# Kernel tuning notes

Hardware: AMD Instinct MI355X
Metric: run time of the kernel (lower is better)

Reference implementation:

```python
import jax, jax.numpy as jnp
import numpy as np

S, B, E = 512, 512, 768

def setup_inputs() -> dict:
    key = jax.random.key(0)
    k1, k2, k3 = jax.random.split(key, 3)
    inputs = jax.random.normal(k1, (S, B, E), dtype=jnp.float32)
    rotation_params = jax.random.normal(k2, (E, E), dtype=jnp.float32)
    entangle_params = jax.random.normal(k3, (E, E), dtype=jnp.float32)
    return {"inputs": inputs, "rotation_params": rotation_params, "entangle_params": entangle_params}

def reference(inputs, rotation_params, entangle_params):
    seq_len, batch, embed_dim = inputs.shape
    # Q/K projections: (S,B,E) @ (E,E) -> (S,B,E)
    q = jnp.einsum('sbe,ef->sbf', inputs, rotation_params.reshape(embed_dim, -1))
    k = jnp.einsum('sbe,ef->sbf', inputs, entangle_params.reshape(embed_dim, -1))
    v = inputs
    # Faithful to the torch code: matmul batches over seq_len, so attention
    # mixes across the BATCH axis -> scores shape (S, B, B).
    scale = 1.0 / jnp.sqrt(jnp.float32(embed_dim))
    scores = jax.nn.softmax(jnp.einsum('sbe,sce->sbc', q, k) * scale, axis=-1)
    return jnp.einsum('sbc,sce->sbe', scores, v)
```

## Files before the change

### kernel.cpp

```cpp
#include <hip/hip_runtime.h>
#include <hip/hip_bf16.h>
#include <math.h>

typedef unsigned short ushort_t;
typedef __attribute__((ext_vector_type(8))) short bf16x8;
typedef __attribute__((ext_vector_type(4))) float f32x4;

#define SCALE 0.03608439182435161f

__device__ __forceinline__ ushort_t f2bf(float f) {
  unsigned u = __float_as_uint(f);
  return (ushort_t)((u + 0x7FFFu + ((u >> 16) & 1u)) >> 16);
}
__device__ __forceinline__ float bf2f(ushort_t h) {
  return __uint_as_float(((unsigned)h) << 16);
}

__device__ __forceinline__ void split4(float4 v, ushort_t* hh, ushort_t* ll) {
  __hip_bfloat162 h01 = __float22bfloat162_rn(make_float2(v.x, v.y));
  __hip_bfloat162 h23 = __float22bfloat162_rn(make_float2(v.z, v.w));
  unsigned u01 = *(unsigned*)&h01, u23 = *(unsigned*)&h23;
  float l0 = v.x - __uint_as_float((u01 & 0xFFFFu) << 16);
  float l1 = v.y - __uint_as_float(u01 & 0xFFFF0000u);
  float l2 = v.z - __uint_as_float((u23 & 0xFFFFu) << 16);
  float l3 = v.w - __uint_as_float(u23 & 0xFFFF0000u);
  __hip_bfloat162 g01 = __float22bfloat162_rn(make_float2(l0, l1));
  __hip_bfloat162 g23 = __float22bfloat162_rn(make_float2(l2, l3));
  *(unsigned*)&hh[0] = u01; *(unsigned*)&hh[2] = u23;
  *(unsigned*)&ll[0] = *(unsigned*)&g01; *(unsigned*)&ll[2] = *(unsigned*)&g23;
}

struct MMP {
  const float* Af;  long aLd;
  const float* Bf;
  const ushort_t* Bhi; const ushort_t* Blo; long bLd;
  ushort_t* Chi; ushort_t* Clo; long cLd;
  int zMode;
  int K;
};

template <int BM>
__global__ __launch_bounds__(256) void mm(MMP P)
{
  __shared__ ushort_t lds[16384];
  ushort_t* Ah = lds;
  ushort_t* Al = lds + 4096;
  ushort_t* Bh = lds + 8192;
  ushort_t* Bl = lds + 12288;

  const int tid = threadIdx.x;
  int bx = blockIdx.x, by = blockIdx.y;
  {
    int nwg = gridDim.x * gridDim.y;
    if ((nwg & 7) == 0) {
      int id = by * gridDim.x + bx;
      int q = nwg >> 3;
      int wid = (id & 7) * q + (id >> 3);
      bx = wid % gridDim.x;
      by = wid / gridDim.x;
    }
  }
  const int m0 = by * 128, n0 = bx * 128;

  const int lane = tid & 63;
  const int wave = tid >> 6;
  const int wm = (wave >> 1) * 64, wn = (wave & 1) * 64;
  const int lr = lane & 15, g = lane >> 4;

  f32x4 acc[4][4];
  #pragma unroll
  for (int i = 0; i < 4; ++i)
    #pragma unroll
    for (int j = 0; j < 4; ++j) {
      f32x4 zv = {0.f, 0.f, 0.f, 0.f};
      acc[i][j] = zv;
    }

  for (int k0 = 0; k0 < P.K; k0 += 32) {
    #pragma unroll
    for (int rep = 0; rep < 4; ++rep) {
      int idx = tid + rep * 256;
      int row = idx >> 3, q = idx & 7;
      float4 v = *(const float4*)(P.Af + (long)(m0 + row) * P.aLd + k0 + q * 4);
      int off = row * 32 + (((q >> 1) ^ ((row >> 1) & 3)) << 3) + ((q & 1) << 2);
      ushort_t hh[4], ll[4];
      split4(v, hh, ll);
      *(uint2*)(Ah + off) = *(uint2*)hh;
      *(uint2*)(Al + off) = *(uint2*)ll;
    }
    if constexpr (BM == 0) {
      #pragma unroll
      for (int rep = 0; rep < 4; ++rep) {
        int idx = tid + rep * 256;
        int row = idx >> 3, q = idx & 7;
        float4 v = *(const float4*)(P.Bf + (long)(n0 + row) * P.bLd + k0 + q * 4);
        int off = row * 32 + (((q >> 1) ^ ((row >> 1) & 3)) << 3) + ((q & 1) << 2);
        ushort_t hh[4], ll[4];
        split4(v, hh, ll);
        *(uint2*)(Bh + off) = *(uint2*)hh;
        *(uint2*)(Bl + off) = *(uint2*)ll;
      }
    } else {
      #pragma unroll
      for (int rep = 0; rep < 2; ++rep) {
        int idx = tid + rep * 256;
        int row = idx >> 2, h8 = idx & 3;
        int off = row * 32 + ((h8 ^ ((row >> 1) & 3)) << 3);
        long gsrc = (long)(n0 + row) * P.bLd + k0 + h8 * 8;
        *(uint4*)(Bh + off) = *(const uint4*)(P.Bhi + gsrc);
        *(uint4*)(Bl + off) = *(const uint4*)(P.Blo + gsrc);
      }
    }
    __syncthreads();

    bf16x8 ar[4], br[4];
    #pragma unroll
    for (int i = 0; i < 4; ++i) {
      int row = wm + i * 16 + lr;
      ar[i] = *(const bf16x8*)(Ah + row * 32 + ((g ^ ((row >> 1) & 3)) << 3));
    }
    #pragma unroll
    for (int j = 0; j < 4; ++j) {
      int row = wn + j * 16 + lr;
      br[j] = *(const bf16x8*)(Bh + row * 32 + ((g ^ ((row >> 1) & 3)) << 3));
    }
    #pragma unroll
    for (int i = 0; i < 4; ++i)
      #pragma unroll
      for (int j = 0; j < 4; ++j)
        acc[i][j] = __builtin_amdgcn_mfma_f32_16x16x32_bf16(ar[i], br[j], acc[i][j], 0, 0, 0);
    #pragma unroll
    for (int j = 0; j < 4; ++j) {
      int row = wn + j * 16 + lr;
      bf16x8 blv = *(const bf16x8*)(Bl + row * 32 + ((g ^ ((row >> 1) & 3)) << 3));
      #pragma unroll
      for (int i = 0; i < 4; ++i)
        acc[i][j] = __builtin_amdgcn_mfma_f32_16x16x32_bf16(ar[i], blv, acc[i][j], 0, 0, 0);
    }
    #pragma unroll
    for (int i = 0; i < 4; ++i) {
      int row = wm + i * 16 + lr;
      bf16x8 alv = *(const bf16x8*)(Al + row * 32 + ((g ^ ((row >> 1) & 3)) << 3));
      #pragma unroll
      for (int j = 0; j < 4; ++j)
        acc[i][j] = __builtin_amdgcn_mfma_f32_16x16x32_bf16(alv, br[j], acc[i][j], 0, 0, 0);
    }
    __syncthreads();
  }

  #pragma unroll
  for (int i = 0; i < 4; ++i) {
    #pragma unroll
    for (int j = 0; j < 4; ++j) {
      int colG = n0 + wn + j * 16 + lr;
      #pragma unroll
      for (int r = 0; r < 4; ++r) {
        int rowG = m0 + wm + i * 16 + g * 4 + r;
        float v = acc[i][j][r];
        ushort_t hi = f2bf(v);
        ushort_t lo = f2bf(v - bf2f(hi));
        long off;
        if (P.zMode) off = (long)(rowG >> 9) * 786432 + (long)(rowG & 511) * 1536 + colG;
        else         off = (long)rowG * P.cLd + colG;
        P.Chi[off] = hi;
        P.Clo[off] = lo;
      }
    }
  }
}

__global__ __launch_bounds__(512, 2) void fsc6(ushort_t* __restrict__ slots,
                                               const float* __restrict__ X)
{
  __shared__ ushort_t lds[73728];
  float* redf = (float*)lds;
  float* reds = (float*)lds + 768;

  const int id = blockIdx.x;
  const int c = id & 7, r = id >> 3;
  const int tile = r & 7;
  const int s = c + ((r >> 3) << 3);
  const int m0 = tile * 64;

  ushort_t* Az = slots + (long)s * 786432;
  const float* Xf = X + (long)s * 393216;

  const int tid = threadIdx.x;
  const int lane = tid & 63;
  const int wave = tid >> 6;
  const int wn = wave * 64;
  const int lr = lane & 15, g = lane >> 4;

  const int ae = tid & 255;
  const int arow = ae >> 2, ah8 = ae & 3;
  const int aoff = arow * 32 + ((ah8 ^ ((arow >> 1) & 3)) << 3);
  const long asrc = (long)(m0 + arow) * 1536 + ah8 * 8 + (tid < 256 ? 0 : 768);
  const int adst = aoff + (tid < 256 ? 0 : 2048);

  f32x4 acc[4][4];
  #pragma unroll
  for (int i = 0; i < 4; ++i)
    #pragma unroll
    for (int j = 0; j < 4; ++j) {
      f32x4 zv = {0.f, 0.f, 0.f, 0.f};
      acc[i][j] = zv;
    }

  float4 bv0, bv1, bv2, bv3, bv4, bv5, bv6, bv7;
  uint4 av;

#define FSC_LOAD(K0)                                                         \
  do {                                                                       \
    av = *(const uint4*)(Az + asrc + (K0));                                  \
    const float* xb = Xf + (K0);                                             \
    bv0 = *(const float4*)(xb + (long)((tid + 0 * 512) >> 3) * 768 + ((tid + 0 * 512) & 7) * 4); \
    bv1 = *(const float4*)(xb + (long)((tid + 1 * 512) >> 3) * 768 + ((tid + 1 * 512) & 7) * 4); \
    bv2 = *(const float4*)(xb + (long)((tid + 2 * 512) >> 3) * 768 + ((tid + 2 * 512) & 7) * 4); \
    bv3 = *(const float4*)(xb + (long)((tid + 3 * 512) >> 3) * 768 + ((tid + 3 * 512) & 7) * 4); \
    bv4 = *(const float4*)(xb + (long)((tid + 4 * 512) >> 3) * 768 + ((tid + 4 * 512) & 7) * 4); \
    bv5 = *(const float4*)(xb + (long)((tid + 5 * 512) >> 3) * 768 + ((tid + 5 * 512) & 7) * 4); \
    bv6 = *(const float4*)(xb + (long)((tid + 6 * 512) >> 3) * 768 + ((tid + 6 * 512) & 7) * 4); \
    bv7 = *(const float4*)(xb + (long)((tid + 7 * 512) >> 3) * 768 + ((tid + 7 * 512) & 7) * 4); \
  } while (0)

#define FSC_WR1(BH, BL, BV, REP)                                             \
  do {                                                                       \
    int idx = tid + (REP) * 512;                                             \
    int row = idx >> 3, q = idx & 7;                                         \
    int off = row * 32 + (((q >> 1) ^ ((row >> 1) & 3)) << 3) + ((q & 1) << 2); \
    ushort_t hh[4], ll[4];                                                   \
    split4(BV, hh, ll);                                                      \
    *(uint2*)((BH) + off) = *(uint2*)hh;                                     \
    *(uint2*)((BL) + off) = *(uint2*)ll;                                     \
  } while (0)

#define FSC_WRITE(B)                                                         \
  do {                                                                       \
    ushort_t* Ab = lds + (B) * 4096;                                         \
    ushort_t* Bhw = lds + 8192 + (B) * 32768;                                \
    ushort_t* Blw = Bhw + 16384;                                             \
    *(uint4*)(Ab + adst) = av;                                               \
    FSC_WR1(Bhw, Blw, bv0, 0); FSC_WR1(Bhw, Blw, bv1, 1);                    \
    FSC_WR1(Bhw, Blw, bv2, 2); FSC_WR1(Bhw, Blw, bv3, 3);                    \
    FSC_WR1(Bhw, Blw, bv4, 4); FSC_WR1(Bhw, Blw, bv5, 5);                    \
    FSC_WR1(Bhw, Blw, bv6, 6); FSC_WR1(Bhw, Blw, bv7, 7);                    \
  } while (0)

  FSC_LOAD(0);
  FSC_WRITE(0);
  __syncthreads();

  for (int t = 0; t < 24; ++t) {
    const int cb = t & 1;
    if (t < 23) FSC_LOAD((t + 1) * 32);
    __builtin_amdgcn_sched_barrier(0);

    const ushort_t* Ab = lds + cb * 4096;
    const ushort_t* Bh = lds + 8192 + cb * 32768;
    const ushort_t* Bl = Bh + 16384;

    bf16x8 arh[4], arl[4], bh[4], bl[4];
    #pragma unroll
    for (int i = 0; i < 4; ++i) {
      int row = i * 16 + lr;
      int off = row * 32 + ((g ^ ((row >> 1) & 3)) << 3);
      arh[i] = *(const bf16x8*)(Ab + off);
      arl[i] = *(const bf16x8*)(Ab + 2048 + off);
    }
    #pragma unroll
    for (int j = 0; j < 4; ++j) {
      int row = wn + j * 16 + lr;
      int off = row * 32 + ((g ^ ((row >> 1) & 3)) << 3);
      bh[j] = *(const bf16x8*)(Bh + off);
      bl[j] = *(const bf16x8*)(Bl + off);
    }
    #pragma unroll
    for (int i = 0; i < 4; ++i)
      #pragma unroll
      for (int j = 0; j < 4; ++j)
        acc[i][j] = __builtin_amdgcn_mfma_f32_16x16x32_bf16(arh[i], bh[j], acc[i][j], 0, 0, 0);
    #pragma unroll
    for (int i = 0; i < 4; ++i)
      #pragma unroll
      for (int j = 0; j < 4; ++j)
        acc[i][j] = __builtin_amdgcn_mfma_f32_16x16x32_bf16(arh[i], bl[j], acc[i][j], 0, 0, 0);
    #pragma unroll
    for (int i = 0; i < 4; ++i)
      #pragma unroll
      for (int j = 0; j < 4; ++j)
        acc[i][j] = __builtin_amdgcn_mfma_f32_16x16x32_bf16(arl[i], bh[j], acc[i][j], 0, 0, 0);

    if (t < 23) FSC_WRITE(1 - cb);
    __syncthreads();
  }

  float mr[4][4];
  #pragma unroll
  for (int i = 0; i < 4; ++i)
    #pragma unroll
    for (int rg = 0; rg < 4; ++rg) {
      float mx = -3.0e38f;
      #pragma unroll
      for (int j = 0; j < 4; ++j) {
        acc[i][j][rg] *= SCALE;
        mx = fmaxf(mx, acc[i][j][rg]);
      }
      #pragma unroll
      for (int off = 8; off >= 1; off >>= 1) mx = fmaxf(mx, __shfl_xor(mx, off, 64));
      if (lr == 0) redf[(i * 16 + g * 4 + rg) * 12 + wave] = mx;
    }
  __syncthreads();
  #pragma unroll
  for (int i = 0; i < 4; ++i)
    #pragma unroll
    for (int rg = 0; rg < 4; ++rg) {
      int row = i * 16 + g * 4 + rg;
      float4 a = *(const float4*)&redf[row * 12];
      float4 b = *(const float4*)&redf[row * 12 + 4];
      mr[i][rg] = fmaxf(fmaxf(fmaxf(a.x, a.y), fmaxf(a.z, a.w)),
                        fmaxf(fmaxf(b.x, b.y), fmaxf(b.z, b.w)));
    }
  #pragma unroll
  for (int i = 0; i < 4; ++i)
    #pragma unroll
    for (int rg = 0; rg < 4; ++rg) {
      float sm = 0.f;
      #pragma unroll
      for (int j = 0; j < 4; ++j) {
        float e = __expf(acc[i][j][rg] - mr[i][rg]);
        acc[i][j][rg] = e;
        sm += e;
      }
      #pragma unroll
      for (int off = 8; off >= 1; off >>= 1) sm += __shfl_xor(sm, off, 64);
      if (lr == 0) reds[(i * 16 + g * 4 + rg) * 12 + wave] = sm;
    }
  __syncthreads();
  #pragma unroll
  for (int i = 0; i < 4; ++i)
    #pragma unroll
    for (int rg = 0; rg < 4; ++rg) {
      int row = i * 16 + g * 4 + rg;
      float4 a = *(const float4*)&reds[row * 12];
      float4 b = *(const float4*)&reds[row * 12 + 4];
      float inv = 1.0f / (a.x + a.y + a.z + a.w + b.x + b.y + b.z + b.w);
      #pragma unroll
      for (int j = 0; j < 4; ++j)
        Az[(long)(m0 + row) * 1536 + wn + j * 16 + lr] = f2bf(acc[i][j][rg] * inv);
    }
}

__global__ __launch_bounds__(768) void pv(float* __restrict__ outp,
                                          const float* __restrict__ X)
{
  __shared__ ushort_t Pa[32768];

  const int id = blockIdx.x;
  const int c = id & 7, r = id >> 3;
  const int tile = r & 7;
  const int s = c + ((r >> 3) << 3);
  const int m0 = tile * 64;

  const ushort_t* Ps = (const ushort_t*)outp + (long)s * 786432;
  const float* Xf = X + (long)s * 393216;

  const int tid = threadIdx.x;
  const int lane = tid & 63;
  const int wave = tid >> 6;
  const int wn = wave * 64;
  const int lr = lane & 15, g = lane >> 4;

  for (int idx = tid; idx < 4096; idx += 768) {
    int row = idx >> 6, h8 = idx & 63;
    int off = row * 512 + ((h8 ^ (row & 7)) << 3);
    *(uint4*)(Pa + off) = *(const uint4*)(Ps + (long)(m0 + row) * 1536 + h8 * 8);
  }
  __syncthreads();

  f32x4 acc[4][4];
  #pragma unroll
  for (int i = 0; i < 4; ++i)
    #pragma unroll
    for (int j = 0; j < 4; ++j) {
      f32x4 zv = {0.f, 0.f, 0.f, 0.f};
      acc[i][j] = zv;
    }

  for (int kk = 0; kk < 16; ++kk) {
    const int k0 = kk * 32;
    bf16x8 ar[4];
    #pragma unroll
    for (int i = 0; i < 4; ++i) {
      int row = i * 16 + lr;
      ar[i] = *(const bf16x8*)(Pa + row * 512 + (((kk * 4 + g) ^ (row & 7)) << 3));
    }
    #pragma unroll
    for (int j = 0; j < 4; ++j) {
      int col = wn + j * 16 + lr;
      float xv[8];
      #pragma unroll
      for (int i = 0; i < 8; ++i)
        xv[i] = Xf[(long)(k0 + g * 8 + i) * 768 + col];
      unsigned w[4];
      #pragma unroll
      for (int p = 0; p < 4; ++p) {
        __hip_bfloat162 hb = __float22bfloat162_rn(make_float2(xv[2 * p], xv[2 * p + 1]));
        w[p] = *(unsigned*)&hb;
      }
      bf16x8 bv = *(bf16x8*)w;
      #pragma unroll
      for (int i = 0; i < 4; ++i)
        acc[i][j] = __builtin_amdgcn_mfma_f32_16x16x32_bf16(ar[i], bv, acc[i][j], 0, 0, 0);
    }
  }

  float* Co = outp + (long)s * 393216;
  #pragma unroll
  for (int i = 0; i < 4; ++i)
    #pragma unroll
    for (int j = 0; j < 4; ++j) {
      int colG = wn + j * 16 + lr;
      #pragma unroll
      for (int rg = 0; rg < 4; ++rg) {
        int rowG = m0 + i * 16 + g * 4 + rg;
        Co[(long)rowG * 768 + colG] = acc[i][j][rg];
      }
    }
}

extern "C" void kernel_launch(void* const* d_in, const int* in_sizes, int n_in,
                              void* d_out, int out_size, void* d_ws, size_t ws_size,
                              hipStream_t stream) {
  const float* X = (const float*)d_in[0];
  const float* R = (const float*)d_in[1];
  const float* W = (const float*)d_in[2];

  ushort_t* Hhi = (ushort_t*)d_ws;
  ushort_t* Hlo = Hhi + 768 * 768;

  {
    MMP p{};
    p.Af = W; p.aLd = 768;
    p.Bf = R; p.bLd = 768;
    p.Chi = Hhi; p.Clo = Hlo; p.cLd = 768; p.zMode = 0;
    p.K = 768;
    mm<0><<<dim3(6, 6), 256, 0, stream>>>(p);
  }
  {
    MMP p{};
    p.Af = X; p.aLd = 768;
    p.Bhi = Hhi; p.Blo = Hlo; p.bLd = 768;
    p.Chi = (ushort_t*)d_out;
    p.Clo = (ushort_t*)d_out + 768;
    p.zMode = 1;
    p.K = 768;
    mm<1><<<dim3(6, 2048), 256, 0, stream>>>(p);
  }
  fsc6<<<dim3(4096), 512, 0, stream>>>((ushort_t*)d_out, X);
  pv<<<dim3(4096), 768, 0, stream>>>((float*)d_out, X);
}
```

Measured before the change: 2.963 ms.

## Load B operand fragments directly from global into registers, dropping LDS staging

New measurement: 3.186 ms. 7.5% more time.

```diff
diff --git a/kernel.cpp b/kernel.cpp
--- a/kernel.cpp
+++ b/kernel.cpp
@@ -169,12 +169,12 @@
   }
 }
 
-__global__ __launch_bounds__(512, 2) void fsc6(ushort_t* __restrict__ slots,
+__global__ __launch_bounds__(512, 2) void fsc7(ushort_t* __restrict__ slots,
                                                const float* __restrict__ X)
 {
-  __shared__ ushort_t lds[73728];
-  float* redf = (float*)lds;
-  float* reds = (float*)lds + 768;
+  __shared__ ushort_t Abuf[8192];
+  float* redf = (float*)Abuf;
+  float* reds = (float*)Abuf + 768;
 
   const int id = blockIdx.x;
   const int c = id & 7, r = id >> 3;
@@ -197,6 +197,8 @@
   const long asrc = (long)(m0 + arow) * 1536 + ah8 * 8 + (tid < 256 ? 0 : 768);
   const int adst = aoff + (tid < 256 ? 0 : 2048);
 
+  const float* xrow0 = Xf + (long)(wn + lr) * 768 + g * 8;
+
   f32x4 acc[4][4];
   #pragma unroll
   for (int i = 0; i < 4; ++i)
@@ -206,60 +208,29 @@
       acc[i][j] = zv;
     }
 
-  float4 bv0, bv1, bv2, bv3, bv4, bv5, bv6, bv7;
+  {
+    uint4 av0 = *(const uint4*)(Az + asrc);
+    *(uint4*)(Abuf + adst) = av0;
+  }
+  __syncthreads();
+
   uint4 av;
-
-#define FSC_LOAD(K0)                                                         \
-  do {                                                                       \
-    av = *(const uint4*)(Az + asrc + (K0));                                  \
-    const float* xb = Xf + (K0);                                             \
-    bv0 = *(const float4*)(xb + (long)((tid + 0 * 512) >> 3) * 768 + ((tid + 0 * 512) & 7) * 4); \
-    bv1 = *(const float4*)(xb + (long)((tid + 1 * 512) >> 3) * 768 + ((tid + 1 * 512) & 7) * 4); \
-    bv2 = *(const float4*)(xb + (long)((tid + 2 * 512) >> 3) * 768 + ((tid + 2 * 512) & 7) * 4); \
-    bv3 = *(const float4*)(xb + (long)((tid + 3 * 512) >> 3) * 768 + ((tid + 3 * 512) & 7) * 4); \
-    bv4 = *(const float4*)(xb + (long)((tid + 4 * 512) >> 3) * 768 + ((tid + 4 * 512) & 7) * 4); \
-    bv5 = *(const float4*)(xb + (long)((tid + 5 * 512) >> 3) * 768 + ((tid + 5 * 512) & 7) * 4); \
-    bv6 = *(const float4*)(xb + (long)((tid + 6 * 512) >> 3) * 768 + ((tid + 6 * 512) & 7) * 4); \
-    bv7 = *(const float4*)(xb + (long)((tid + 7 * 512) >> 3) * 768 + ((tid + 7 * 512) & 7) * 4); \
-  } while (0)
-
-#define FSC_WR1(BH, BL, BV, REP)                                             \
-  do {                                                                       \
-    int idx = tid + (REP) * 512;                                             \
-    int row = idx >> 3, q = idx & 7;                                         \
-    int off = row * 32 + (((q >> 1) ^ ((row >> 1) & 3)) << 3) + ((q & 1) << 2); \
-    ushort_t hh[4], ll[4];                                                   \
-    split4(BV, hh, ll);                                                      \
-    *(uint2*)((BH) + off) = *(uint2*)hh;                                     \
-    *(uint2*)((BL) + off) = *(uint2*)ll;                                     \
-  } while (0)
-
-#define FSC_WRITE(B)                                                         \
-  do {                                                                       \
-    ushort_t* Ab = lds + (B) * 4096;                                         \
-    ushort_t* Bhw = lds + 8192 + (B) * 32768;                                \
-    ushort_t* Blw = Bhw + 16384;                                             \
-    *(uint4*)(Ab + adst) = av;                                               \
-    FSC_WR1(Bhw, Blw, bv0, 0); FSC_WR1(Bhw, Blw, bv1, 1);                    \
-    FSC_WR1(Bhw, Blw, bv2, 2); FSC_WR1(Bhw, Blw, bv3, 3);                    \
-    FSC_WR1(Bhw, Blw, bv4, 4); FSC_WR1(Bhw, Blw, bv5, 5);                    \
-    FSC_WR1(Bhw, Blw, bv6, 6); FSC_WR1(Bhw, Blw, bv7, 7);                    \
-  } while (0)
-
-  FSC_LOAD(0);
-  FSC_WRITE(0);
-  __syncthreads();
-
   for (int t = 0; t < 24; ++t) {
     const int cb = t & 1;
-    if (t < 23) FSC_LOAD((t + 1) * 32);
+    const int k0 = t * 32;
+
+    float4 bvf[4][2];
+    #pragma unroll
+    for (int j = 0; j < 4; ++j) {
+      const float* xp = xrow0 + (long)j * 16 * 768 + k0;
+      bvf[j][0] = *(const float4*)xp;
+      bvf[j][1] = *(const float4*)(xp + 4);
+    }
+    if (t < 23) av = *(const uint4*)(Az + asrc + (t + 1) * 32);
     __builtin_amdgcn_sched_barrier(0);
 
-    const ushort_t* Ab = lds + cb * 4096;
-    const ushort_t* Bh = lds + 8192 + cb * 32768;
-    const ushort_t* Bl = Bh + 16384;
-
-    bf16x8 arh[4], arl[4], bh[4], bl[4];
+    const ushort_t* Ab = Abuf + cb * 4096;
+    bf16x8 arh[4], arl[4];
     #pragma unroll
     for (int i = 0; i < 4; ++i) {
       int row = i * 16 + lr;
@@ -267,13 +238,16 @@
       arh[i] = *(const bf16x8*)(Ab + off);
       arl[i] = *(const bf16x8*)(Ab + 2048 + off);
     }
-    #pragma unroll
-    for (int j = 0; j < 4; ++j) {
-      int row = wn + j * 16 + lr;
-      int off = row * 32 + ((g ^ ((row >> 1) & 3)) << 3);
-      bh[j] = *(const bf16x8*)(Bh + off);
-      bl[j] = *(const bf16x8*)(Bl + off);
-    }
+    bf16x8 bh[4], bl[4];
+    #pragma unroll
+    for (int j = 0; j < 4; ++j) {
+      ushort_t hh[8], ll[8];
+      split4(bvf[j][0], &hh[0], &ll[0]);
+      split4(bvf[j][1], &hh[4], &ll[4]);
+      bh[j] = *(bf16x8*)hh;
+      bl[j] = *(bf16x8*)ll;
+    }
+
     #pragma unroll
     for (int i = 0; i < 4; ++i)
       #pragma unroll
@@ -290,7 +264,7 @@
       for (int j = 0; j < 4; ++j)
         acc[i][j] = __builtin_amdgcn_mfma_f32_16x16x32_bf16(arl[i], bh[j], acc[i][j], 0, 0, 0);
 
-    if (t < 23) FSC_WRITE(1 - cb);
+    if (t < 23) *(uint4*)(Abuf + (1 - cb) * 4096 + adst) = av;
     __syncthreads();
   }
 
@@ -456,6 +430,6 @@
     p.K = 768;
     mm<1><<<dim3(6, 2048), 256, 0, stream>>>(p);
   }
-  fsc6<<<dim3(4096), 512, 0, stream>>>((ushort_t*)d_out, X);
+  fsc7<<<dim3(4096), 512, 0, stream>>>((ushort_t*)d_out, X);
   pv<<<dim3(4096), 768, 0, stream>>>((float*)d_out, X);
 }
```

## Double the score-softmax kernel's row tile to 128 and single-buffer LDS

Applied to the files above, without the earlier changes.

Result: slower. 3.121 ms (+5.3%).

```diff
diff --git a/kernel.cpp b/kernel.cpp
--- a/kernel.cpp
+++ b/kernel.cpp
@@ -169,18 +169,22 @@
   }
 }
 
-__global__ __launch_bounds__(512, 2) void fsc6(ushort_t* __restrict__ slots,
+__global__ __launch_bounds__(512, 2) void fsc8(ushort_t* __restrict__ slots,
                                                const float* __restrict__ X)
 {
-  __shared__ ushort_t lds[73728];
+  __shared__ ushort_t lds[40960];
+  ushort_t* Bh = lds;
+  ushort_t* Bl = lds + 16384;
+  ushort_t* Ah = lds + 32768;
+  ushort_t* Al = lds + 36864;
   float* redf = (float*)lds;
-  float* reds = (float*)lds + 768;
+  float* reds = (float*)lds + 1536;
 
   const int id = blockIdx.x;
-  const int c = id & 7, r = id >> 3;
-  const int tile = r & 7;
-  const int s = c + ((r >> 3) << 3);
-  const int m0 = tile * 64;
+  const int c = id & 7, t0 = id >> 3;
+  const int tile = t0 & 3;
+  const int s = c + ((t0 >> 2) << 3);
+  const int m0 = tile * 128;
 
   ushort_t* Az = slots + (long)s * 786432;
   const float* Xf = X + (long)s * 393216;
@@ -191,15 +195,13 @@
   const int wn = wave * 64;
   const int lr = lane & 15, g = lane >> 4;
 
-  const int ae = tid & 255;
-  const int arow = ae >> 2, ah8 = ae & 3;
+  const int arow = tid >> 2, ah8 = tid & 3;
   const int aoff = arow * 32 + ((ah8 ^ ((arow >> 1) & 3)) << 3);
-  const long asrc = (long)(m0 + arow) * 1536 + ah8 * 8 + (tid < 256 ? 0 : 768);
-  const int adst = aoff + (tid < 256 ? 0 : 2048);
-
-  f32x4 acc[4][4];
-  #pragma unroll
-  for (int i = 0; i < 4; ++i)
+  const long asrc = (long)(m0 + arow) * 1536 + ah8 * 8;
+
+  f32x4 acc[8][4];
+  #pragma unroll
+  for (int i = 0; i < 8; ++i)
     #pragma unroll
     for (int j = 0; j < 4; ++j) {
       f32x4 zv = {0.f, 0.f, 0.f, 0.f};
@@ -207,11 +209,12 @@
     }
 
   float4 bv0, bv1, bv2, bv3, bv4, bv5, bv6, bv7;
-  uint4 av;
-
-#define FSC_LOAD(K0)                                                         \
+  uint4 avh, avl;
+
+#define F8_LOAD(K0)                                                          \
   do {                                                                       \
-    av = *(const uint4*)(Az + asrc + (K0));                                  \
+    avh = *(const uint4*)(Az + asrc + (K0));                                 \
+    avl = *(const uint4*)(Az + asrc + (K0) + 768);                           \
     const float* xb = Xf + (K0);                                             \
     bv0 = *(const float4*)(xb + (long)((tid + 0 * 512) >> 3) * 768 + ((tid + 0 * 512) & 7) * 4); \
     bv1 = *(const float4*)(xb + (long)((tid + 1 * 512) >> 3) * 768 + ((tid + 1 * 512) & 7) * 4); \
@@ -223,80 +226,73 @@
     bv7 = *(const float4*)(xb + (long)((tid + 7 * 512) >> 3) * 768 + ((tid + 7 * 512) & 7) * 4); \
   } while (0)
 
-#define FSC_WR1(BH, BL, BV, REP)                                             \
+#define F8_WR1(BV, REP)                                                      \
   do {                                                                       \
     int idx = tid + (REP) * 512;                                             \
     int row = idx >> 3, q = idx & 7;                                         \
     int off = row * 32 + (((q >> 1) ^ ((row >> 1) & 3)) << 3) + ((q & 1) << 2); \
     ushort_t hh[4], ll[4];                                                   \
     split4(BV, hh, ll);                                                      \
-    *(uint2*)((BH) + off) = *(uint2*)hh;                                     \
-    *(uint2*)((BL) + off) = *(uint2*)ll;                                     \
+    *(uint2*)(Bh + off) = *(uint2*)hh;                                       \
+    *(uint2*)(Bl + off) = *(uint2*)ll;                                       \
   } while (0)
 
-#define FSC_WRITE(B)                                                         \
+#define F8_WRITE()                                                           \
   do {                                                                       \
-    ushort_t* Ab = lds + (B) * 4096;                                         \
-    ushort_t* Bhw = lds + 8192 + (B) * 32768;                                \
-    ushort_t* Blw = Bhw + 16384;                                             \
-    *(uint4*)(Ab + adst) = av;                                               \
-    FSC_WR1(Bhw, Blw, bv0, 0); FSC_WR1(Bhw, Blw, bv1, 1);                    \
-    FSC_WR1(Bhw, Blw, bv2, 2); FSC_WR1(Bhw, Blw, bv3, 3);                    \
-    FSC_WR1(Bhw, Blw, bv4, 4); FSC_WR1(Bhw, Blw, bv5, 5);                    \
-    FSC_WR1(Bhw, Blw, bv6, 6); FSC_WR1(Bhw, Blw, bv7, 7);                    \
+    *(uint4*)(Ah + aoff) = avh;                                              \
+    *(uint4*)(Al + aoff) = avl;                                              \
+    F8_WR1(bv0, 0); F8_WR1(bv1, 1); F8_WR1(bv2, 2); F8_WR1(bv3, 3);          \
+    F8_WR1(bv4, 4); F8_WR1(bv5, 5); F8_WR1(bv6, 6); F8_WR1(bv7, 7);          \
   } while (0)
 
-  FSC_LOAD(0);
-  FSC_WRITE(0);
+  F8_LOAD(0);
+  F8_WRITE();
   __syncthreads();
 
   for (int t = 0; t < 24; ++t) {
-    const int cb = t & 1;
-    if (t < 23) FSC_LOAD((t + 1) * 32);
+    if (t < 23) F8_LOAD((t + 1) * 32);
     __builtin_amdgcn_sched_barrier(0);
 
-    const ushort_t* Ab = lds + cb * 4096;
-    const ushort_t* Bh = lds + 8192 + cb * 32768;
-    const ushort_t* Bl = Bh + 16384;
-
-    bf16x8 arh[4], arl[4], bh[4], bl[4];
-    #pragma unroll
-    for (int i = 0; i < 4; ++i) {
-      int row = i * 16 + lr;
-      int off = row * 32 + ((g ^ ((row >> 1) & 3)) << 3);
-      arh[i] = *(const bf16x8*)(Ab + off);
-      arl[i] = *(const bf16x8*)(Ab + 2048 + off);
-    }
+    bf16x8 bhf[4], blf[4], arh[8];
     #pragma unroll
     for (int j = 0; j < 4; ++j) {
       int row = wn + j * 16 + lr;
       int off = row * 32 + ((g ^ ((row >> 1) & 3)) << 3);
-      bh[j] = *(const bf16x8*)(Bh + off);
-      bl[j] = *(const bf16x8*)(Bl + off);
-    }
-    #pragma unroll
-    for (int i = 0; i < 4; ++i)
-      #pragma unroll
-      for (int j = 0; j < 4; ++j)
-        acc[i][j] = __builtin_amdgcn_mfma_f32_16x16x32_bf16(arh[i], bh[j], acc[i][j], 0, 0, 0);
-    #pragma unroll
-    for (int i = 0; i < 4; ++i)
-      #pragma unroll
-      for (int j = 0; j < 4; ++j)
-        acc[i][j] = __builtin_amdgcn_mfma_f32_16x16x32_bf16(arh[i], bl[j], acc[i][j], 0, 0, 0);
-    #pragma unroll
-    for (int i = 0; i < 4; ++i)
-      #pragma unroll
-      for (int j = 0; j < 4; ++j)
-        acc[i][j] = __builtin_amdgcn_mfma_f32_16x16x32_bf16(arl[i], bh[j], acc[i][j], 0, 0, 0);
-
-    if (t < 23) FSC_WRITE(1 - cb);
+      bhf[j] = *(const bf16x8*)(Bh + off);
+      blf[j] = *(const bf16x8*)(Bl + off);
+    }
+    #pragma unroll
+    for (int i = 0; i < 8; ++i) {
+      int row = i * 16 + lr;
+      arh[i] = *(const bf16x8*)(Ah + row * 32 + ((g ^ ((row >> 1) & 3)) << 3));
+    }
+    #pragma unroll
+    for (int i = 0; i < 8; ++i)
+      #pragma unroll
+      for (int j = 0; j < 4; ++j)
+        acc[i][j] = __builtin_amdgcn_mfma_f32_16x16x32_bf16(arh[i], bhf[j], acc[i][j], 0, 0, 0);
+    #pragma unroll
+    for (int i = 0; i < 8; ++i)
+      #pragma unroll
+      for (int j = 0; j < 4; ++j)
+        acc[i][j] = __builtin_amdgcn_mfma_f32_16x16x32_bf16(arh[i], blf[j], acc[i][j], 0, 0, 0);
+    #pragma unroll
+    for (int i = 0; i < 8; ++i) {
+      int row = i * 16 + lr;
+      bf16x8 arl = *(const bf16x8*)(Al + row * 32 + ((g ^ ((row >> 1) & 3)) << 3));
+      #pragma unroll
+      for (int j = 0; j < 4; ++j)
+        acc[i][j] = __builtin_amdgcn_mfma_f32_16x16x32_bf16(arl, bhf[j], acc[i][j], 0, 0, 0);
+    }
+
     __syncthreads();
-  }
-
-  float mr[4][4];
-  #pragma unroll
-  for (int i = 0; i < 4; ++i)
+    if (t < 23) F8_WRITE();
+    __syncthreads();
+  }
+
+  float mr[8][4];
+  #pragma unroll
+  for (int i = 0; i < 8; ++i)
     #pragma unroll
     for (int rg = 0; rg < 4; ++rg) {
       float mx = -3.0e38f;
@@ -311,7 +307,7 @@
     }
   __syncthreads();
   #pragma unroll
-  for (int i = 0; i < 4; ++i)
+  for (int i = 0; i < 8; ++i)
     #pragma unroll
     for (int rg = 0; rg < 4; ++rg) {
       int row = i * 16 + g * 4 + rg;
@@ -321,7 +317,7 @@
                         fmaxf(fmaxf(b.x, b.y), fmaxf(b.z, b.w)));
     }
   #pragma unroll
-  for (int i = 0; i < 4; ++i)
+  for (int i = 0; i < 8; ++i)
     #pragma unroll
     for (int rg = 0; rg < 4; ++rg) {
       float sm = 0.f;
@@ -337,7 +333,7 @@
     }
   __syncthreads();
   #pragma unroll
-  for (int i = 0; i < 4; ++i)
+  for (int i = 0; i < 8; ++i)
     #pragma unroll
     for (int rg = 0; rg < 4; ++rg) {
       int row = i * 16 + g * 4 + rg;
@@ -456,6 +452,6 @@
     p.K = 768;
     mm<1><<<dim3(6, 2048), 256, 0, stream>>>(p);
   }
-  fsc6<<<dim3(4096), 512, 0, stream>>>((ushort_t*)d_out, X);
+  fsc8<<<dim3(2048), 512, 0, stream>>>((ushort_t*)d_out, X);
   pv<<<dim3(4096), 768, 0, stream>>>((float*)d_out, X);
 }
```

## Fuse softmax and PV matmul into one kernel keeping probabilities in LDS

Applied to the files above, without the earlier changes.

Measured after the change: 2.773 ms. 1.07x faster.

```diff
diff --git a/kernel.cpp b/kernel.cpp
--- a/kernel.cpp
+++ b/kernel.cpp
@@ -169,12 +169,13 @@
   }
 }
 
-__global__ __launch_bounds__(512, 2) void fsc6(ushort_t* __restrict__ slots,
-                                               const float* __restrict__ X)
+__global__ __launch_bounds__(512, 1) void fpv(ushort_t* __restrict__ slots,
+                                              const float* __restrict__ X)
 {
   __shared__ ushort_t lds[73728];
   float* redf = (float*)lds;
   float* reds = (float*)lds + 768;
+  ushort_t* Pl = lds + 8192;
 
   const int id = blockIdx.x;
   const int c = id & 7, r = id >> 3;
@@ -345,87 +346,64 @@
       float4 b = *(const float4*)&reds[row * 12 + 4];
       float inv = 1.0f / (a.x + a.y + a.z + a.w + b.x + b.y + b.z + b.w);
       #pragma unroll
-      for (int j = 0; j < 4; ++j)
-        Az[(long)(m0 + row) * 1536 + wn + j * 16 + lr] = f2bf(acc[i][j][rg] * inv);
-    }
-}
-
-__global__ __launch_bounds__(768) void pv(float* __restrict__ outp,
-                                          const float* __restrict__ X)
-{
-  __shared__ ushort_t Pa[32768];
-
-  const int id = blockIdx.x;
-  const int c = id & 7, r = id >> 3;
-  const int tile = r & 7;
-  const int s = c + ((r >> 3) << 3);
-  const int m0 = tile * 64;
-
-  const ushort_t* Ps = (const ushort_t*)outp + (long)s * 786432;
-  const float* Xf = X + (long)s * 393216;
-
-  const int tid = threadIdx.x;
-  const int lane = tid & 63;
-  const int wave = tid >> 6;
-  const int wn = wave * 64;
-  const int lr = lane & 15, g = lane >> 4;
-
-  for (int idx = tid; idx < 4096; idx += 768) {
-    int row = idx >> 6, h8 = idx & 63;
-    int off = row * 512 + ((h8 ^ (row & 7)) << 3);
-    *(uint4*)(Pa + off) = *(const uint4*)(Ps + (long)(m0 + row) * 1536 + h8 * 8);
-  }
+      for (int j = 0; j < 4; ++j) {
+        int col = wn + j * 16 + lr;
+        Pl[row * 512 + (((col >> 3) ^ (row & 7)) << 3) + (col & 7)] =
+            f2bf(acc[i][j][rg] * inv);
+      }
+    }
   __syncthreads();
 
-  f32x4 acc[4][4];
-  #pragma unroll
-  for (int i = 0; i < 4; ++i)
-    #pragma unroll
-    for (int j = 0; j < 4; ++j) {
-      f32x4 zv = {0.f, 0.f, 0.f, 0.f};
-      acc[i][j] = zv;
-    }
-
-  for (int kk = 0; kk < 16; ++kk) {
-    const int k0 = kk * 32;
-    bf16x8 ar[4];
-    #pragma unroll
-    for (int i = 0; i < 4; ++i) {
-      int row = i * 16 + lr;
-      ar[i] = *(const bf16x8*)(Pa + row * 512 + (((kk * 4 + g) ^ (row & 7)) << 3));
-    }
-    #pragma unroll
-    for (int j = 0; j < 4; ++j) {
-      int col = wn + j * 16 + lr;
-      float xv[8];
-      #pragma unroll
-      for (int i = 0; i < 8; ++i)
-        xv[i] = Xf[(long)(k0 + g * 8 + i) * 768 + col];
-      unsigned w[4];
-      #pragma unroll
-      for (int p = 0; p < 4; ++p) {
-        __hip_bfloat162 hb = __float22bfloat162_rn(make_float2(xv[2 * p], xv[2 * p + 1]));
-        w[p] = *(unsigned*)&hb;
-      }
-      bf16x8 bv = *(bf16x8*)w;
-      #pragma unroll
-      for (int i = 0; i < 4; ++i)
-        acc[i][j] = __builtin_amdgcn_mfma_f32_16x16x32_bf16(ar[i], bv, acc[i][j], 0, 0, 0);
-    }
-  }
-
-  float* Co = outp + (long)s * 393216;
-  #pragma unroll
-  for (int i = 0; i < 4; ++i)
-    #pragma unroll
-    for (int j = 0; j < 4; ++j) {
-      int colG = wn + j * 16 + lr;
-      #pragma unroll
-      for (int rg = 0; rg < 4; ++rg) {
-        int rowG = m0 + i * 16 + g * 4 + rg;
-        Co[(long)rowG * 768 + colG] = acc[i][j][rg];
-      }
-    }
+  float* Co = (float*)slots + (long)s * 393216;
+  #pragma unroll
+  for (int cg = 0; cg < 2; ++cg) {
+    const int cbase = wave * 96 + cg * 48;
+    f32x4 acc2[4][3];
+    #pragma unroll
+    for (int i = 0; i < 4; ++i)
+      #pragma unroll
+      for (int j = 0; j < 3; ++j) {
+        f32x4 zv = {0.f, 0.f, 0.f, 0.f};
+        acc2[i][j] = zv;
+      }
+    for (int kk = 0; kk < 16; ++kk) {
+      bf16x8 pa[4];
+      #pragma unroll
+      for (int i = 0; i < 4; ++i) {
+        int row = i * 16 + lr;
+        pa[i] = *(const bf16x8*)(Pl + row * 512 + (((kk * 4 + g) ^ (row & 7)) << 3));
+      }
+      #pragma unroll
+      for (int j = 0; j < 3; ++j) {
+        int col = cbase + j * 16 + lr;
+        float xv[8];
+        #pragma unroll
+        for (int ii = 0; ii < 8; ++ii)
+          xv[ii] = Xf[(long)(kk * 32 + g * 8 + ii) * 768 + col];
+        unsigned w[4];
+        #pragma unroll
+        for (int p = 0; p < 4; ++p) {
+          __hip_bfloat162 hb = __float22bfloat162_rn(make_float2(xv[2 * p], xv[2 * p + 1]));
+          w[p] = *(unsigned*)&hb;
+        }
+        bf16x8 bv = *(bf16x8*)w;
+        #pragma unroll
+        for (int i = 0; i < 4; ++i)
+          acc2[i][j] = __builtin_amdgcn_mfma_f32_16x16x32_bf16(pa[i], bv, acc2[i][j], 0, 0, 0);
+      }
+    }
+    #pragma unroll
+    for (int i = 0; i < 4; ++i)
+      #pragma unroll
+      for (int j = 0; j < 3; ++j) {
+        int colG = cbase + j * 16 + lr;
+        #pragma unroll
+        for (int rg = 0; rg < 4; ++rg) {
+          int rowG = m0 + i * 16 + g * 4 + rg;
+          Co[(long)rowG * 768 + colG] = acc2[i][j][rg];
+        }
+      }
+  }
 }
 
 extern "C" void kernel_launch(void* const* d_in, const int* in_sizes, int n_in,
@@ -456,6 +434,5 @@
     p.K = 768;
     mm<1><<<dim3(6, 2048), 256, 0, stream>>>(p);
   }
-  fsc6<<<dim3(4096), 512, 0, stream>>>((ushort_t*)d_out, X);
-  pv<<<dim3(4096), 768, 0, stream>>>((float*)d_out, X);
-}
+  fpv<<<dim3(4096), 512, 0, stream>>>((ushort_t*)d_out, X);
+}
```
